# Performance work log

Measured on AMD Instinct MI355X. Metric: run time of the kernel, lower is better.

## Reference

```python
import jax, jax.numpy as jnp
import numpy as np

V, E, H, M, B, S = 32000, 512, 1024, 256, 2, 1024
GC = 24  # smear_gate_channels = min(24, embedding_dim)


def setup_inputs() -> dict:
    key = jax.random.key(0)
    ks = jax.random.split(key, 20)
    s = 0.02
    return {
        "input_ids": jax.random.randint(ks[0], (B, S), 0, V),
        "emb": jax.random.normal(ks[1], (V, E)) * s,
        "W_ih": jax.random.normal(ks[2], (3 * H, E)) * s,
        "W_hh": jax.random.normal(ks[3], (3 * H, H)) * s,
        "b_ih": jax.random.normal(ks[4], (3 * H,)) * s,
        "b_hh": jax.random.normal(ks[5], (3 * H,)) * s,
        "Wq": jax.random.normal(ks[6], (M, H)) * s,
        "bq": jax.random.normal(ks[7], (M,)) * s,
        "Wk": jax.random.normal(ks[8], (M, H)) * s,
        "bk": jax.random.normal(ks[9], (M,)) * s,
        "Wg": jax.random.normal(ks[10], (1, H)) * s,
        "bg": jax.random.normal(ks[11], (1,)) * s,
        "Whe": jax.random.normal(ks[12], (E, H)) * s,
        "bhe": jax.random.normal(ks[13], (E,)) * s,
        "out_bias": jax.random.normal(ks[14], (V,)) * s,
        "memory_scale": jnp.float32(6.0),
        "smear_W": jax.random.normal(ks[15], (1, GC)) * s,
        "smear_lambda": jax.random.normal(ks[16], (1,)) * 0.1,
    }


def forward(input_ids, emb, W_ih, W_hh, b_ih, b_hh, Wq, bq, Wk, bk, Wg, bg,
            Whe, bhe, out_bias, memory_scale, smear_W, smear_lambda):
    x = emb[input_ids]  # (B,S,E)
    # smear: gated copy of previous token embedding into current
    sg = smear_lambda * jax.nn.sigmoid(x[:, 1:, :GC] @ smear_W.T)  # (B,S-1,1)
    x = jnp.concatenate([x[:, :1], x[:, 1:] + sg * x[:, :-1]], axis=1)
    # GRU (PyTorch gate order r,z,n); precompute input projections
    xg = x @ W_ih.T + b_ih  # (B,S,3H)

    def step(h, xg_t):
        xr, xz, xn = jnp.split(xg_t, 3, axis=-1)
        hg = h @ W_hh.T + b_hh
        hr, hz, hn = jnp.split(hg, 3, axis=-1)
        r = jax.nn.sigmoid(xr + hr)
        z = jax.nn.sigmoid(xz + hz)
        n = jnp.tanh(xn + r * hn)
        h_new = (1.0 - z) * n + z * h
        return h_new, h_new

    h0 = jnp.zeros((x.shape[0], H), dtype=x.dtype)
    _, states = jax.lax.scan(step, h0, jnp.swapaxes(xg, 0, 1))
    states = jnp.swapaxes(states, 0, 1)  # (B,S,H); dropout is identity at eval
    # tied output projection
    base_logits = (states @ Whe.T + bhe) @ emb.T + out_bias  # (B,S,V)
    q = states @ Wq.T + bq  # (B,S,M)
    k = states @ Wk.T + bk
    scores = jnp.einsum("bsm,btm->bst", q, k) / jnp.sqrt(jnp.float32(M))
    mask = jnp.tril(jnp.ones((S, S), dtype=bool), k=-1)[None]  # (1,S,S)
    scores = jnp.where(mask, scores, jnp.finfo(scores.dtype).min)
    attn = jax.nn.softmax(scores, axis=-1) * mask
    attn = attn / jnp.maximum(attn.sum(axis=-1, keepdims=True), 1e-6)
    g = jax.nn.sigmoid(states @ Wg.T + bg)  # (B,S,1)
    gated = attn * (g * memory_scale)  # (B,S,S)
    # scatter_add gated attention into vocab logits at input_ids positions
    b_idx = jnp.arange(B)[:, None, None]
    s_idx = jnp.arange(S)[None, :, None]
    v_idx = input_ids[:, None, :]  # broadcasts to (B,S,S)
    base_logits = base_logits.at[b_idx, s_idx, v_idx].add(gated)
    return base_logits


def reference(input_ids, emb, W_ih, W_hh, b_ih, b_hh, Wq, bq, Wk, bk, Wg, bg,
              Whe, bhe, out_bias, memory_scale, smear_W, smear_lambda):
    return forward(input_ids, emb, W_ih, W_hh, b_ih, b_hh, Wq, bq, Wk, bk,
                   Wg, bg, Whe, bhe, out_bias, memory_scale, smear_W, smear_lambda)
```

## Files before the change

### kernel.cpp

```cpp
#include <hip/hip_runtime.h>
#include <stdint.h>

#define V_ 32000
#define E_ 512
#define H_ 1024
#define M_ 256
#define B_ 2
#define S_ 1024
#define GC_ 24

typedef unsigned short u16;
typedef unsigned int u32;
typedef unsigned long long u64;

typedef __attribute__((ext_vector_type(8))) short short8;
typedef __attribute__((ext_vector_type(4))) float floatx4;
typedef __attribute__((ext_vector_type(2))) float floatx2;
typedef __attribute__((ext_vector_type(2))) _Float16 halfx2;

__device__ __forceinline__ float bf2f(u16 u){ return __uint_as_float(((u32)u) << 16); }
__device__ __forceinline__ float bflo(u32 u){ return __uint_as_float(u << 16); }
__device__ __forceinline__ float bfhi(u32 u){ return __uint_as_float(u & 0xffff0000u); }
__device__ __forceinline__ u16 f2bf(float f){
  u32 u = __float_as_uint(f);
  u32 r = (u + 0x7fffu + ((u >> 16) & 1u)) >> 16;
  return (u16)r;
}
__device__ __forceinline__ float sigm(float x){ return 1.f / (1.f + __expf(-x)); }

__device__ __forceinline__ float dot2f16(u32 a, u32 b, float c){
#if __has_builtin(__builtin_amdgcn_fdot2)
  return __builtin_amdgcn_fdot2(__builtin_bit_cast(halfx2, a),
                                __builtin_bit_cast(halfx2, b), c, false);
#else
  halfx2 av = __builtin_bit_cast(halfx2, a);
  halfx2 bv = __builtin_bit_cast(halfx2, b);
  return fmaf((float)av.y, (float)bv.y, fmaf((float)av.x, (float)bv.x, c));
#endif
}

__device__ __forceinline__ void gload_lds16(const void* g, void* l){
  __builtin_amdgcn_global_load_lds(
      (const __attribute__((address_space(1))) void*)g,
      (__attribute__((address_space(3))) void*)l, 16, 0, 0);
}

__global__ __launch_bounds__(64) void detect_kernel(const u32* __restrict__ emb,
    int* __restrict__ flag, float* __restrict__ scal,
    const void* __restrict__ lam, const void* __restrict__ ms)
{
  int lane = threadIdx.x;
  int c = 0;
  for (int i = lane; i < 256; i += 64){
    u32 w = emb[i];
    float a = fabsf(__uint_as_float((w & 0xffffu) << 16));
    if (a > 1e-5f && a < 1.0f) c++;
  }
  #pragma unroll
  for (int o = 32; o; o >>= 1) c += __shfl_down(c, o, 64);
  if (lane == 0){
    int isf32 = (c < 128) ? 1 : 0;
    *flag = isf32;
    if (isf32) scal[0] = ((const float*)lam)[0];
    else {
      float v = bf2f(((const u16*)lam)[0]);
      scal[0] = (fabsf(v) <= 4.0f) ? v : ((const float*)lam)[0];
    }
    if (isf32) scal[1] = ((const float*)ms)[0];
    else {
      u16 a = ((const u16*)ms)[0];
      float v = bf2f(a);
      scal[1] = (a != 0 && fabsf(v) > 1e-4f && fabsf(v) < 1e4f) ? v : ((const float*)ms)[0];
    }
  }
}

struct ConvArgs { const void* s[15]; };

#define CONV_TOTAL 22191385
__global__ __launch_bounds__(256) void convall_kernel(ConvArgs a, char* __restrict__ ws,
                                                      const int* __restrict__ flag)
{
  static const int    ns[15]    = {16384000, 1572864, 3145728, 262144, 262144, 1024,
                                   524288, 3072, 3072, 256, 256, 1, 512, 32000, 24};
  static const size_t doffs[15] = {33280, 32801280, 35947008, 42238464, 42762752,
                                   43287040, 43289088, 44337664, 44343808, 44349952,
                                   44350464, 44350976, 44351232, 44352256, 44416512};
  int gid = blockIdx.x * 256 + threadIdx.x;
  if (gid >= CONV_TOTAL) return;
  int isf32 = *flag;
  int seg = -1, r = gid;
  #pragma unroll
  for (int k = 0; k < 15; k++){
    if (seg < 0){ if (r < ns[k]) seg = k; else r -= ns[k]; }
  }
  const void* src = a.s[seg];
  u16* dst = (u16*)(ws + doffs[seg]);
  if (seg == 2){
    float v = isf32 ? ((const float*)src)[r] : bf2f(((const u16*)src)[r]);
    dst[r] = __builtin_bit_cast(u16, (_Float16)v);
  } else {
    dst[r] = isf32 ? f2bf(((const float*)src)[r]) : ((const u16*)src)[r];
  }
}

__global__ __launch_bounds__(64) void smear_kernel(const int* __restrict__ ids,
    const u16* __restrict__ emb, const u16* __restrict__ smW,
    const float* __restrict__ scal, u16* __restrict__ xs)
{
  int row = blockIdx.x;
  int t = row & (S_ - 1);
  int lane = threadIdx.x;
  int id = ids[row];
  const u16* er = emb + (size_t)id * E_;
  float sg = 0.f;
  if (t > 0){
    float p = 0.f;
    if (lane < GC_) p = bf2f(er[lane]) * bf2f(smW[lane]);
    #pragma unroll
    for (int o = 32; o; o >>= 1) p += __shfl_down(p, o, 64);
    float dot = __shfl(p, 0, 64);
    sg = scal[0] * sigm(dot);
  }
  uint4 cur = ((const uint4*)er)[lane];
  uint4 outv = cur;
  if (t > 0){
    const u16* ep = emb + (size_t)ids[row - 1] * E_;
    uint4 prv = ((const uint4*)ep)[lane];
    const u16* cu = (const u16*)&cur;
    const u16* pu = (const u16*)&prv;
    u16* po = (u16*)&outv;
    #pragma unroll
    for (int j = 0; j < 8; j++) po[j] = f2bf(bf2f(cu[j]) + sg * bf2f(pu[j]));
  }
  ((uint4*)(xs + (size_t)row * E_))[lane] = outv;
}

template<bool OUT_BF16>
__global__ __launch_bounds__(256) void gemm_bt(
    const u16* __restrict__ A, const u16* __restrict__ Bm,
    const u16* __restrict__ bias, void* __restrict__ Cout,
    int K, int Ndim)
{
  int wave = threadIdx.x >> 6, lane = threadIdx.x & 63;
  int wm = wave >> 1, wn = wave & 1;
  int m0 = blockIdx.y * 128 + wm * 64;
  int n0 = blockIdx.x * 128 + wn * 64;
  int lrow = lane & 15, lq = lane >> 4;
  floatx4 acc[4][4];
  #pragma unroll
  for (int i = 0; i < 4; i++)
    #pragma unroll
    for (int j = 0; j < 4; j++) acc[i][j] = (floatx4)0.f;
  const u16* Ab = A + (size_t)(m0 + lrow) * K + lq * 8;
  const u16* Bb = Bm + (size_t)(n0 + lrow) * K + lq * 8;
  for (int k0 = 0; k0 < K; k0 += 32){
    short8 af[4], bfr[4];
    #pragma unroll
    for (int tt = 0; tt < 4; tt++)
      af[tt] = *(const short8*)(Ab + (size_t)tt * 16 * K + k0);
    #pragma unroll
    for (int tt = 0; tt < 4; tt++)
      bfr[tt] = *(const short8*)(Bb + (size_t)tt * 16 * K + k0);
    #pragma unroll
    for (int im = 0; im < 4; im++)
      #pragma unroll
      for (int in = 0; in < 4; in++)
        acc[im][in] = __builtin_amdgcn_mfma_f32_16x16x32_bf16(af[im], bfr[in], acc[im][in], 0, 0, 0);
  }
  #pragma unroll
  for (int in = 0; in < 4; in++){
    int n = n0 + in * 16 + lrow;
    float bv = bf2f(bias[n]);
    #pragma unroll
    for (int im = 0; im < 4; im++){
      int mb = m0 + im * 16 + lq * 4;
      #pragma unroll
      for (int r = 0; r < 4; r++){
        float v = acc[im][in][r] + bv;
        size_t off = (size_t)(mb + r) * Ndim + n;
        if (OUT_BF16) ((u16*)Cout)[off] = f2bf(v);
        else          ((float*)Cout)[off] = v;
      }
    }
  }
}

__global__ __launch_bounds__(256) void gemm_v(
    const u16* __restrict__ A, const u16* __restrict__ Bm,
    const u16* __restrict__ bias, float* __restrict__ Cout,
    int K, int Ndim)
{
  __shared__ u16 la[128 * 32];
  __shared__ u16 lb[128 * 32];
  int wave = threadIdx.x >> 6, lane = threadIdx.x & 63;
  int wm = wave >> 1, wn = wave & 1;
  int tm0 = blockIdx.x * 128, tn0 = blockIdx.y * 128;
  int m0 = tm0 + wm * 64;
  int n0 = tn0 + wn * 64;
  int lrow = lane & 15, lq = lane >> 4;
  floatx4 acc[4][4];
  #pragma unroll
  for (int i = 0; i < 4; i++)
    #pragma unroll
    for (int j = 0; j < 4; j++) acc[i][j] = (floatx4)0.f;

  const int o = wave * 1024 + lane * 16;
  for (int k0 = 0; k0 < K; k0 += 32){
    #pragma unroll
    for (int j = 0; j < 2; j++){
      int oo = o + j * 4096;
      int row = oo >> 6;
      int ce  = (oo & 63) >> 1;
      gload_lds16(&A[(size_t)(tm0 + row) * K + k0 + ce],  &la[(wave * 1024 + j * 4096) >> 1]);
      gload_lds16(&Bm[(size_t)(tn0 + row) * K + k0 + ce], &lb[(wave * 1024 + j * 4096) >> 1]);
    }
    __syncthreads();
    short8 af[4], bfr[4];
    #pragma unroll
    for (int tt = 0; tt < 4; tt++)
      af[tt] = *(const short8*)&la[(wm * 64 + tt * 16 + lrow) * 32 + lq * 8];
    #pragma unroll
    for (int tt = 0; tt < 4; tt++)
      bfr[tt] = *(const short8*)&lb[(wn * 64 + tt * 16 + lrow) * 32 + lq * 8];
    #pragma unroll
    for (int im = 0; im < 4; im++)
      #pragma unroll
      for (int in = 0; in < 4; in++)
        acc[im][in] = __builtin_amdgcn_mfma_f32_16x16x32_bf16(af[im], bfr[in], acc[im][in], 0, 0, 0);
    __syncthreads();
  }
  #pragma unroll
  for (int in = 0; in < 4; in++){
    int n = n0 + in * 16 + lrow;
    float bv = bf2f(bias[n]);
    #pragma unroll
    for (int im = 0; im < 4; im++){
      int mb = m0 + im * 16 + lq * 4;
      #pragma unroll
      for (int r = 0; r < 4; r++)
        Cout[(size_t)(mb + r) * Ndim + n] = acc[im][in][r] + bv;
    }
  }
}

__global__ __launch_bounds__(1024) void gru_kernel(
    const float* __restrict__ xg, const u16* __restrict__ W_hh,
    const u16* __restrict__ b_hh, u32* __restrict__ hslot,
    u16* __restrict__ states, const int* __restrict__ ids, int* __restrict__ sorted)
{
  __shared__ int arr[S_];
  if (blockIdx.x >= 64){
    int b = blockIdx.x - 64, tid = threadIdx.x;
    arr[tid] = (ids[b * S_ + tid] << 11) | tid;
    __syncthreads();
    for (int k = 2; k <= S_; k <<= 1){
      for (int j = k >> 1; j > 0; j >>= 1){
        int ixj = tid ^ j;
        if (ixj > tid){
          int a = arr[tid], c = arr[ixj];
          bool dir = (tid & k) == 0;
          if (dir ? (a > c) : (a < c)){ arr[tid] = c; arr[ixj] = a; }
        }
        __syncthreads();
      }
    }
    sorted[b * S_ + tid] = arr[tid];
    return;
  }

  const int b = blockIdx.x >> 5;
  const int ibase = (blockIdx.x & 31) * 32;
  const int tid = threadIdx.x;
  const int kg = tid >> 5;
  const int il = tid & 31;
  const int i = ibase + il;
  const int w = tid >> 6;

  __shared__ u32   lds_hpk[2][H_ / 2];
  __shared__ float red[3][16][32];

  uint4 Wv[3][4];
  #pragma unroll
  for (int g = 0; g < 3; g++){
    const uint4* p = (const uint4*)(W_hh + ((size_t)(g * H_ + i)) * H_ + kg * 32);
    #pragma unroll
    for (int q = 0; q < 4; q++) Wv[g][q] = p[q];
  }

  float ho = 0.f, xr0 = 0.f, xz0 = 0.f, xn0 = 0.f, bh0 = 0.f, bh1 = 0.f, bh2 = 0.f;
  if (tid < 32){
    bh0 = bf2f(b_hh[ibase + tid]);
    bh1 = bf2f(b_hh[H_ + ibase + tid]);
    bh2 = bf2f(b_hh[2 * H_ + ibase + tid]);
    size_t base = ((size_t)(b * S_)) * 3072 + ibase + tid;
    xr0 = xg[base]; xz0 = xg[base + 1024]; xn0 = xg[base + 2048];
  }

  for (int t = 0; t < S_; t++){
    const int p = t & 1;
    if (tid < 512){
      const u64* rp = (const u64*)(hslot + ((size_t)((p ^ 1) * B_ + b)) * H_) + tid;
      const u32 tg = (u32)t;
      u64 u0;
      do {
        u0 = __hip_atomic_load(rp, __ATOMIC_RELAXED, __HIP_MEMORY_SCOPE_AGENT);
      } while ((((u32)(u0 >> 16) & 0xffffu) != tg) | (((u32)(u0 >> 48)) != tg));
      lds_hpk[p][tid] = ((u32)u0 & 0xffffu) | (((u32)(u0 >> 32)) << 16);
    }
    __syncthreads();
    const u32* hp = &lds_hpk[p][kg * 16];
    float pr = 0.f, pz = 0.f, pn = 0.f;
    #pragma unroll
    for (int q = 0; q < 4; q++){
      uint4 wr = Wv[0][q], wz = Wv[1][q], wn4 = Wv[2][q];
      u32 cr[4] = {wr.x, wr.y, wr.z, wr.w};
      u32 cz[4] = {wz.x, wz.y, wz.z, wz.w};
      u32 cn[4] = {wn4.x, wn4.y, wn4.z, wn4.w};
      #pragma unroll
      for (int e = 0; e < 4; e++){
        u32 h2 = hp[q * 4 + e];
        pr = dot2f16(cr[e], h2, pr);
        pz = dot2f16(cz[e], h2, pz);
        pn = dot2f16(cn[e], h2, pn);
      }
    }
    pr += __shfl_xor(pr, 32, 64);
    pz += __shfl_xor(pz, 32, 64);
    pn += __shfl_xor(pn, 32, 64);
    if ((tid & 63) < 32){
      red[0][w][il] = pr; red[1][w][il] = pz; red[2][w][il] = pn;
    }
    __syncthreads();
    if (tid < 32){
      __builtin_amdgcn_s_setprio(1);
      float hr = 0.f, hz = 0.f, hn = 0.f;
      #pragma unroll
      for (int ww = 0; ww < 16; ww++){
        hr += red[0][ww][tid]; hz += red[1][ww][tid]; hn += red[2][ww][tid];
      }
      float r = sigm(xr0 + hr + bh0);
      float z = sigm(xz0 + hz + bh1);
      float xx = xn0 + r * (hn + bh2);
      float ax = fabsf(xx);
      float et = __expf(-2.f * ax);
      float n = copysignf((1.f - et) * __builtin_amdgcn_rcpf(1.f + et), xx);
      float hnew = (1.f - z) * n + z * ho;
      ho = hnew;
      u16 h16 = __builtin_bit_cast(u16, (_Float16)hnew);
      u32 tgv = (((u32)(t + 1)) << 16) | (u32)h16;
      __hip_atomic_store(&hslot[((size_t)(p * B_ + b)) * H_ + ibase + tid], tgv,
                         __ATOMIC_RELAXED, __HIP_MEMORY_SCOPE_AGENT);
      __builtin_amdgcn_s_setprio(0);
      states[((size_t)(b * S_ + t)) * H_ + ibase + tid] = f2bf(hnew);
      if (t + 1 < S_){
        size_t base = ((size_t)(b * S_ + t + 1)) * 3072 + ibase + tid;
        xr0 = xg[base]; xz0 = xg[base + 1024]; xn0 = xg[base + 2048];
      }
    }
  }
}

__global__ __launch_bounds__(256) void gk_kernel(const u16* __restrict__ states,
    const u16* __restrict__ Wg, const u16* __restrict__ bg, float* __restrict__ gws)
{
  int row = blockIdx.x * 4 + (threadIdx.x >> 6);
  int lane = threadIdx.x & 63;
  const u16* sr = states + (size_t)row * H_;
  float p = 0.f;
  #pragma unroll
  for (int j = 0; j < 16; j++){
    int c = j * 64 + lane;
    p += bf2f(sr[c]) * bf2f(Wg[c]);
  }
  #pragma unroll
  for (int o = 32; o; o >>= 1) p += __shfl_xor(p, o, 64);
  if (lane == 0) gws[row] = sigm(p + bf2f(bg[0]));
}

__global__ __launch_bounds__(256) void attn_scatter_kernel(
    const float* __restrict__ scores, const float* __restrict__ gws,
    const float* __restrict__ scal, const int* __restrict__ sorted,
    float* __restrict__ out)
{
  int s = blockIdx.x, b = blockIdx.y;
  if (s == 0) return;
  int tid = threadIdx.x;
  __shared__ float grow[S_];
  __shared__ int   sb[S_];
  __shared__ float rbm[4], rbs[4];
  const float* srow = scores + ((size_t)(b * S_ + s)) * S_;
  #pragma unroll
  for (int r = 0; r < 4; r++) sb[tid + 256 * r] = sorted[b * S_ + tid + 256 * r];
  float myS[4];
  float lmax = -1e30f;
  #pragma unroll
  for (int r = 0; r < 4; r++){
    int t = tid + 256 * r;
    if (t < s){
      float d = srow[t] * 0.0625f;
      myS[r] = d;
      lmax = fmaxf(lmax, d);
    }
  }
  #pragma unroll
  for (int o = 32; o; o >>= 1) lmax = fmaxf(lmax, __shfl_xor(lmax, o, 64));
  if ((tid & 63) == 0) rbm[tid >> 6] = lmax;
  __syncthreads();
  float gmax = fmaxf(fmaxf(rbm[0], rbm[1]), fmaxf(rbm[2], rbm[3]));
  float lsum = 0.f;
  #pragma unroll
  for (int r = 0; r < 4; r++){
    int t = tid + 256 * r;
    if (t < s){ myS[r] = __expf(myS[r] - gmax); lsum += myS[r]; }
  }
  #pragma unroll
  for (int o = 32; o; o >>= 1) lsum += __shfl_xor(lsum, o, 64);
  if ((tid & 63) == 0) rbs[tid >> 6] = lsum;
  __syncthreads();
  float gsum = rbs[0] + rbs[1] + rbs[2] + rbs[3];
  float fac = gws[b * S_ + s] * scal[1] / gsum;
  #pragma unroll
  for (int r = 0; r < 4; r++){
    int t = tid + 256 * r;
    if (t < s) grow[t] = myS[r] * fac;
  }
  __syncthreads();
  float* orow = out + ((size_t)(b * S_ + s)) * V_;
  #pragma unroll
  for (int r = 0; r < 4; r++){
    int e = tid + 256 * r;
    int pk = sb[e];
    int v = pk >> 11;
    if (e > 0 && (sb[e - 1] >> 11) == v) continue;
    float sum = 0.f; bool any = false;
    for (int j = e; j < S_; j++){
      int pj = sb[j];
      if ((pj >> 11) != v) break;
      int t = pj & 2047;
      if (t < s){ sum += grow[t]; any = true; }
    }
    if (any) orow[v] += sum;
  }
}

extern "C" void kernel_launch(void* const* d_in, const int* in_sizes, int n_in,
                              void* d_out, int out_size, void* d_ws, size_t ws_size,
                              hipStream_t stream)
{
  const int*  ids   = (const int*)d_in[0];
  const void* emb   = d_in[1];
  const void* W_ih  = d_in[2];
  const void* W_hh  = d_in[3];
  const void* b_ih  = d_in[4];
  const void* b_hh  = d_in[5];
  const void* Wq    = d_in[6];
  const void* bq    = d_in[7];
  const void* Wk    = d_in[8];
  const void* bk    = d_in[9];
  const void* Wg    = d_in[10];
  const void* bg    = d_in[11];
  const void* Whe   = d_in[12];
  const void* bhe   = d_in[13];
  const void* obias = d_in[14];
  const void* ms    = d_in[15];
  const void* smW   = d_in[16];
  const void* lam   = d_in[17];
  (void)in_sizes; (void)n_in; (void)out_size; (void)ws_size;

  char* ws = (char*)d_ws;
  int*   flag   = (int*)(ws + 0);
  float* scal   = (float*)(ws + 256);
  u32*   hslot  = (u32*)(ws + 512);
  u16*   zbias  = (u16*)(ws + 16896);
  u16*   c_emb  = (u16*)(ws + 33280);
  u16*   c_Wih  = (u16*)(ws + 32801280);
  u16*   c_Whh  = (u16*)(ws + 35947008);
  u16*   c_Wq   = (u16*)(ws + 42238464);
  u16*   c_Wk   = (u16*)(ws + 42762752);
  u16*   c_Wg   = (u16*)(ws + 43287040);
  u16*   c_Whe  = (u16*)(ws + 43289088);
  u16*   c_bih  = (u16*)(ws + 44337664);
  u16*   c_bhh  = (u16*)(ws + 44343808);
  u16*   c_bq   = (u16*)(ws + 44349952);
  u16*   c_bk   = (u16*)(ws + 44350464);
  u16*   c_bg   = (u16*)(ws + 44350976);
  u16*   c_bhe  = (u16*)(ws + 44351232);
  u16*   c_ob   = (u16*)(ws + 44352256);
  u16*   c_smW  = (u16*)(ws + 44416512);
  u16*   xs     = (u16*)(ws + 44416768);
  float* xg     = (float*)(ws + 46513920);
  u16*   states = (u16*)(ws + 71679744);
  u16*   hs     = (u16*)(ws + 75874048);
  u16*   qb     = (u16*)(ws + 77971200);
  u16*   kb     = (u16*)(ws + 79019776);
  float* gws    = (float*)(ws + 80068352);
  int*   sorted = (int*)(ws + 88465152);
  float* scores = xg;
  float* out = (float*)d_out;

  hipMemsetAsync(hslot, 0, 16384, stream);
  hipMemsetAsync(zbias, 0, 2048, stream);
  detect_kernel<<<dim3(1), dim3(64), 0, stream>>>((const u32*)emb, flag, scal, lam, ms);

  ConvArgs ca;
  ca.s[0] = emb;  ca.s[1] = W_ih; ca.s[2] = W_hh; ca.s[3] = Wq;   ca.s[4] = Wk;
  ca.s[5] = Wg;   ca.s[6] = Whe;  ca.s[7] = b_ih; ca.s[8] = b_hh; ca.s[9] = bq;
  ca.s[10] = bk;  ca.s[11] = bg;  ca.s[12] = bhe; ca.s[13] = obias; ca.s[14] = smW;
  convall_kernel<<<dim3((CONV_TOTAL + 255) / 256), dim3(256), 0, stream>>>(ca, ws, flag);

  smear_kernel<<<dim3(B_ * S_), dim3(64), 0, stream>>>(ids, c_emb, c_smW, scal, xs);
  gemm_bt<false><<<dim3(3072 / 128, 2048 / 128), dim3(256), 0, stream>>>(xs, c_Wih, c_bih, (void*)xg, E_, 3072);
  gru_kernel<<<dim3(66), dim3(1024), 0, stream>>>(xg, c_Whh, c_bhh, hslot, states, ids, sorted);
  gemm_bt<true><<<dim3(512 / 128, 16), dim3(256), 0, stream>>>(states, c_Whe, c_bhe, (void*)hs, H_, 512);
  gemm_bt<true><<<dim3(256 / 128, 16), dim3(256), 0, stream>>>(states, c_Wq, c_bq, (void*)qb, H_, 256);
  gemm_bt<true><<<dim3(256 / 128, 16), dim3(256), 0, stream>>>(states, c_Wk, c_bk, (void*)kb, H_, 256);
  gemm_bt<false><<<dim3(S_ / 128, S_ / 128), dim3(256), 0, stream>>>(qb, kb, zbias, (void*)scores, M_, S_);
  gemm_bt<false><<<dim3(S_ / 128, S_ / 128), dim3(256), 0, stream>>>(qb + (size_t)S_ * M_, kb + (size_t)S_ * M_,
                                                                     zbias, (void*)(scores + (size_t)S_ * S_), M_, S_);
  gk_kernel<<<dim3(512), dim3(256), 0, stream>>>(states, c_Wg, c_bg, gws);
  gemm_v<<<dim3(16, V_ / 128), dim3(256), 0, stream>>>(hs, c_emb, c_ob, out, E_, V_);
  attn_scatter_kernel<<<dim3(S_, B_), dim3(256), 0, stream>>>(scores, gws, scal, sorted, out);
}
```

Before: 2.484 ms.

## Fuse GRU with downstream GEMMs in persistent megakernel overlapping via progress counters

Merges the GRU recurrence, bitonic sort, output-projection, Q/K projection, vocab-logit and score GEMMs into one persistent kernel. The GRU blocks bump per-128-step counters, and 190 extra worker blocks wait on those counters to run dependent GEMM tiles while the recurrence is still going. The goal is to hide the large vocab GEMM and the projections behind the latency-bound sequential GRU. In exchange, the GEMM tiles now read operands straight from global memory with no LDS staging, and the workers spin-wait, which risks contending with the GRU blocks for CUs and memory bandwidth. It also relies on every block being co-resident to avoid deadlock.

```diff
diff --git a/kernel.cpp b/kernel.cpp
--- a/kernel.cpp
+++ b/kernel.cpp
@@ -39,12 +39,6 @@
 #endif
 }
 
-__device__ __forceinline__ void gload_lds16(const void* g, void* l){
-  __builtin_amdgcn_global_load_lds(
-      (const __attribute__((address_space(1))) void*)g,
-      (__attribute__((address_space(3))) void*)l, 16, 0, 0);
-}
-
 __global__ __launch_bounds__(64) void detect_kernel(const u32* __restrict__ emb,
     int* __restrict__ flag, float* __restrict__ scal,
     const void* __restrict__ lam, const void* __restrict__ ms)
@@ -186,16 +180,11 @@
   }
 }
 
-__global__ __launch_bounds__(256) void gemm_v(
-    const u16* __restrict__ A, const u16* __restrict__ Bm,
-    const u16* __restrict__ bias, float* __restrict__ Cout,
-    int K, int Ndim)
-{
-  __shared__ u16 la[128 * 32];
-  __shared__ u16 lb[128 * 32];
-  int wave = threadIdx.x >> 6, lane = threadIdx.x & 63;
+__device__ void tile_gemm(const u16* __restrict__ A, const u16* __restrict__ Bm,
+                          const u16* __restrict__ bias, void* __restrict__ Cout,
+                          int K, int Ndim, int tm0, int tn0, int wave, int lane, int outbf)
+{
   int wm = wave >> 1, wn = wave & 1;
-  int tm0 = blockIdx.x * 128, tn0 = blockIdx.y * 128;
   int m0 = tm0 + wm * 64;
   int n0 = tn0 + wn * 64;
   int lrow = lane & 15, lq = lane >> 4;
@@ -204,31 +193,21 @@
   for (int i = 0; i < 4; i++)
     #pragma unroll
     for (int j = 0; j < 4; j++) acc[i][j] = (floatx4)0.f;
-
-  const int o = wave * 1024 + lane * 16;
+  const u16* Ab = A + (size_t)(m0 + lrow) * K + lq * 8;
+  const u16* Bb = Bm + (size_t)(n0 + lrow) * K + lq * 8;
   for (int k0 = 0; k0 < K; k0 += 32){
-    #pragma unroll
-    for (int j = 0; j < 2; j++){
-      int oo = o + j * 4096;
-      int row = oo >> 6;
-      int ce  = (oo & 63) >> 1;
-      gload_lds16(&A[(size_t)(tm0 + row) * K + k0 + ce],  &la[(wave * 1024 + j * 4096) >> 1]);
-      gload_lds16(&Bm[(size_t)(tn0 + row) * K + k0 + ce], &lb[(wave * 1024 + j * 4096) >> 1]);
-    }
-    __syncthreads();
     short8 af[4], bfr[4];
     #pragma unroll
     for (int tt = 0; tt < 4; tt++)
-      af[tt] = *(const short8*)&la[(wm * 64 + tt * 16 + lrow) * 32 + lq * 8];
+      af[tt] = *(const short8*)(Ab + (size_t)tt * 16 * K + k0);
     #pragma unroll
     for (int tt = 0; tt < 4; tt++)
-      bfr[tt] = *(const short8*)&lb[(wn * 64 + tt * 16 + lrow) * 32 + lq * 8];
+      bfr[tt] = *(const short8*)(Bb + (size_t)tt * 16 * K + k0);
     #pragma unroll
     for (int im = 0; im < 4; im++)
       #pragma unroll
       for (int in = 0; in < 4; in++)
         acc[im][in] = __builtin_amdgcn_mfma_f32_16x16x32_bf16(af[im], bfr[in], acc[im][in], 0, 0, 0);
-    __syncthreads();
   }
   #pragma unroll
   for (int in = 0; in < 4; in++){
@@ -238,40 +217,110 @@
     for (int im = 0; im < 4; im++){
       int mb = m0 + im * 16 + lq * 4;
       #pragma unroll
-      for (int r = 0; r < 4; r++)
-        Cout[(size_t)(mb + r) * Ndim + n] = acc[im][in][r] + bv;
-    }
-  }
-}
-
-__global__ __launch_bounds__(1024) void gru_kernel(
-    const float* __restrict__ xg, const u16* __restrict__ W_hh,
-    const u16* __restrict__ b_hh, u32* __restrict__ hslot,
-    u16* __restrict__ states, const int* __restrict__ ids, int* __restrict__ sorted)
-{
+      for (int r = 0; r < 4; r++){
+        float v = acc[im][in][r] + bv;
+        size_t off = (size_t)(mb + r) * Ndim + n;
+        if (outbf) ((u16*)Cout)[off] = f2bf(v);
+        else       ((float*)Cout)[off] = v;
+      }
+    }
+  }
+}
+
+struct MegaArgs {
+  const float* xg; const u16* Whh; const u16* bhh; u32* hslot; u16* states;
+  const int* ids; int* sorted;
+  const u16* Whe; const u16* bhe; u16* hs;
+  const u16* Wq;  const u16* bq;  u16* qb;
+  const u16* Wk;  const u16* bk;  u16* kb;
+  const u16* emb; const u16* ob;  float* out;
+  const u16* zbias; float* scores;
+  u32* ctr;
+};
+
+__global__ __launch_bounds__(1024) void mega_kernel(MegaArgs a)
+{
+  const int tid = threadIdx.x;
+
   __shared__ int arr[S_];
-  if (blockIdx.x >= 64){
-    int b = blockIdx.x - 64, tid = threadIdx.x;
-    arr[tid] = (ids[b * S_ + tid] << 11) | tid;
+  if (blockIdx.x >= 64 && blockIdx.x < 66){
+    int b = blockIdx.x - 64;
+    arr[tid] = (a.ids[b * S_ + tid] << 11) | tid;
     __syncthreads();
     for (int k = 2; k <= S_; k <<= 1){
       for (int j = k >> 1; j > 0; j >>= 1){
         int ixj = tid ^ j;
         if (ixj > tid){
-          int a = arr[tid], c = arr[ixj];
+          int x = arr[tid], c = arr[ixj];
           bool dir = (tid & k) == 0;
-          if (dir ? (a > c) : (a < c)){ arr[tid] = c; arr[ixj] = a; }
+          if (dir ? (x > c) : (x < c)){ arr[tid] = c; arr[ixj] = x; }
         }
         __syncthreads();
       }
     }
-    sorted[b * S_ + tid] = arr[tid];
+    a.sorted[b * S_ + tid] = arr[tid];
+    return;
+  }
+
+  if (blockIdx.x >= 66){
+    const int wid = blockIdx.x - 66;
+    const int qt = tid >> 8;
+    const int qtid = tid & 255;
+    const int wave = qtid >> 6, lane = qtid & 63;
+    u32* prog = a.ctr;
+    u32* hsd  = a.ctr + 16;
+    u32* qkvt = a.ctr + 32;
+    for (int q = wid; q < 1072; q += 190){
+      int type, mt = 0, nq = 0, sbb = 0, si = 0, sj0 = 0;
+      if (q < 1040){
+        int c = q / 130, r = q - c * 130;
+        if (r < 2){ type = 0; mt = c + 8 * r; }
+        else if (r < 4){ type = 1; mt = c + 8 * (r - 2); }
+        else { type = 2; int rr = r - 4; mt = c + 8 * (rr / 63); nq = rr - (rr / 63) * 63; }
+      } else {
+        type = 3; int r = q - 1040; sbb = r >> 4;
+        int qq = r & 15; si = qq >> 1; sj0 = (qq & 1) * 4;
+      }
+      if (tid == 0){
+        if (type <= 1){
+          while (__hip_atomic_load(&prog[mt], __ATOMIC_ACQUIRE, __HIP_MEMORY_SCOPE_AGENT) < 32u)
+            __builtin_amdgcn_s_sleep(8);
+        } else if (type == 2){
+          while (__hip_atomic_load(&hsd[mt], __ATOMIC_ACQUIRE, __HIP_MEMORY_SCOPE_AGENT) == 0u)
+            __builtin_amdgcn_s_sleep(8);
+        } else {
+          while (__hip_atomic_load(qkvt, __ATOMIC_ACQUIRE, __HIP_MEMORY_SCOPE_AGENT) < 16u)
+            __builtin_amdgcn_s_sleep(8);
+        }
+      }
+      __syncthreads();
+      if (type == 0){
+        tile_gemm(a.states, a.Whe, a.bhe, a.hs, H_, 512, mt * 128, qt * 128, wave, lane, 1);
+      } else if (type == 1){
+        if (qt < 2) tile_gemm(a.states, a.Wq, a.bq, a.qb, H_, M_, mt * 128, qt * 128, wave, lane, 1);
+        else        tile_gemm(a.states, a.Wk, a.bk, a.kb, H_, M_, mt * 128, (qt - 2) * 128, wave, lane, 1);
+      } else if (type == 2){
+        int ntile = nq * 4 + qt;
+        if (ntile < 250)
+          tile_gemm(a.hs, a.emb, a.ob, a.out, E_, V_, mt * 128, ntile * 128, wave, lane, 0);
+      } else {
+        int j = sj0 + qt;
+        tile_gemm(a.qb + (size_t)sbb * S_ * M_, a.kb + (size_t)sbb * S_ * M_, a.zbias,
+                  a.scores + (size_t)sbb * S_ * S_, M_, S_, si * 128, j * 128, wave, lane, 0);
+      }
+      __syncthreads();
+      if (tid == 0){
+        if (type == 0)
+          __hip_atomic_store(&hsd[mt], 1u, __ATOMIC_RELEASE, __HIP_MEMORY_SCOPE_AGENT);
+        else if (type == 1)
+          __hip_atomic_fetch_add(qkvt, 1u, __ATOMIC_RELEASE, __HIP_MEMORY_SCOPE_AGENT);
+      }
+    }
     return;
   }
 
   const int b = blockIdx.x >> 5;
   const int ibase = (blockIdx.x & 31) * 32;
-  const int tid = threadIdx.x;
   const int kg = tid >> 5;
   const int il = tid & 31;
   const int i = ibase + il;
@@ -283,24 +332,24 @@
   uint4 Wv[3][4];
   #pragma unroll
   for (int g = 0; g < 3; g++){
-    const uint4* p = (const uint4*)(W_hh + ((size_t)(g * H_ + i)) * H_ + kg * 32);
+    const uint4* p = (const uint4*)(a.Whh + ((size_t)(g * H_ + i)) * H_ + kg * 32);
     #pragma unroll
     for (int q = 0; q < 4; q++) Wv[g][q] = p[q];
   }
 
   float ho = 0.f, xr0 = 0.f, xz0 = 0.f, xn0 = 0.f, bh0 = 0.f, bh1 = 0.f, bh2 = 0.f;
   if (tid < 32){
-    bh0 = bf2f(b_hh[ibase + tid]);
-    bh1 = bf2f(b_hh[H_ + ibase + tid]);
-    bh2 = bf2f(b_hh[2 * H_ + ibase + tid]);
+    bh0 = bf2f(a.bhh[ibase + tid]);
+    bh1 = bf2f(a.bhh[H_ + ibase + tid]);
+    bh2 = bf2f(a.bhh[2 * H_ + ibase + tid]);
     size_t base = ((size_t)(b * S_)) * 3072 + ibase + tid;
-    xr0 = xg[base]; xz0 = xg[base + 1024]; xn0 = xg[base + 2048];
+    xr0 = a.xg[base]; xz0 = a.xg[base + 1024]; xn0 = a.xg[base + 2048];
   }
 
   for (int t = 0; t < S_; t++){
     const int p = t & 1;
     if (tid < 512){
-      const u64* rp = (const u64*)(hslot + ((size_t)((p ^ 1) * B_ + b)) * H_) + tid;
+      const u64* rp = (const u64*)(a.hslot + ((size_t)((p ^ 1) * B_ + b)) * H_) + tid;
       const u32 tg = (u32)t;
       u64 u0;
       do {
@@ -349,13 +398,16 @@
       ho = hnew;
       u16 h16 = __builtin_bit_cast(u16, (_Float16)hnew);
       u32 tgv = (((u32)(t + 1)) << 16) | (u32)h16;
-      __hip_atomic_store(&hslot[((size_t)(p * B_ + b)) * H_ + ibase + tid], tgv,
+      __hip_atomic_store(&a.hslot[((size_t)(p * B_ + b)) * H_ + ibase + tid], tgv,
                          __ATOMIC_RELAXED, __HIP_MEMORY_SCOPE_AGENT);
       __builtin_amdgcn_s_setprio(0);
-      states[((size_t)(b * S_ + t)) * H_ + ibase + tid] = f2bf(hnew);
+      a.states[((size_t)(b * S_ + t)) * H_ + ibase + tid] = f2bf(hnew);
+      if (((t + 1) & 127) == 0 && tid == 0)
+        __hip_atomic_fetch_add(&a.ctr[b * 8 + (t >> 7)], 1u,
+                               __ATOMIC_RELEASE, __HIP_MEMORY_SCOPE_AGENT);
       if (t + 1 < S_){
         size_t base = ((size_t)(b * S_ + t + 1)) * 3072 + ibase + tid;
-        xr0 = xg[base]; xz0 = xg[base + 1024]; xn0 = xg[base + 2048];
+        xr0 = a.xg[base]; xz0 = a.xg[base + 1024]; xn0 = a.xg[base + 2048];
       }
     }
   }
@@ -473,6 +525,7 @@
   float* scal   = (float*)(ws + 256);
   u32*   hslot  = (u32*)(ws + 512);
   u16*   zbias  = (u16*)(ws + 16896);
+  u32*   ctr    = (u32*)(ws + 20480);
   u16*   c_emb  = (u16*)(ws + 33280);
   u16*   c_Wih  = (u16*)(ws + 32801280);
   u16*   c_Whh  = (u16*)(ws + 35947008);
@@ -501,6 +554,7 @@
 
   hipMemsetAsync(hslot, 0, 16384, stream);
   hipMemsetAsync(zbias, 0, 2048, stream);
+  hipMemsetAsync(ctr, 0, 256, stream);
   detect_kernel<<<dim3(1), dim3(64), 0, stream>>>((const u32*)emb, flag, scal, lam, ms);
 
   ConvArgs ca;
@@ -511,14 +565,18 @@
 
   smear_kernel<<<dim3(B_ * S_), dim3(64), 0, stream>>>(ids, c_emb, c_smW, scal, xs);
   gemm_bt<false><<<dim3(3072 / 128, 2048 / 128), dim3(256), 0, stream>>>(xs, c_Wih, c_bih, (void*)xg, E_, 3072);
-  gru_kernel<<<dim3(66), dim3(1024), 0, stream>>>(xg, c_Whh, c_bhh, hslot, states, ids, sorted);
-  gemm_bt<true><<<dim3(512 / 128, 16), dim3(256), 0, stream>>>(states, c_Whe, c_bhe, (void*)hs, H_, 512);
-  gemm_bt<true><<<dim3(256 / 128, 16), dim3(256), 0, stream>>>(states, c_Wq, c_bq, (void*)qb, H_, 256);
-  gemm_bt<true><<<dim3(256 / 128, 16), dim3(256), 0, stream>>>(states, c_Wk, c_bk, (void*)kb, H_, 256);
-  gemm_bt<false><<<dim3(S_ / 128, S_ / 128), dim3(256), 0, stream>>>(qb, kb, zbias, (void*)scores, M_, S_);
-  gemm_bt<false><<<dim3(S_ / 128, S_ / 128), dim3(256), 0, stream>>>(qb + (size_t)S_ * M_, kb + (size_t)S_ * M_,
-                                                                     zbias, (void*)(scores + (size_t)S_ * S_), M_, S_);
+
+  MegaArgs ma;
+  ma.xg = xg;        ma.Whh = c_Whh;  ma.bhh = c_bhh;  ma.hslot = hslot;  ma.states = states;
+  ma.ids = ids;      ma.sorted = sorted;
+  ma.Whe = c_Whe;    ma.bhe = c_bhe;  ma.hs = hs;
+  ma.Wq = c_Wq;      ma.bq = c_bq;    ma.qb = qb;
+  ma.Wk = c_Wk;      ma.bk = c_bk;    ma.kb = kb;
+  ma.emb = c_emb;    ma.ob = c_ob;    ma.out = out;
+  ma.zbias = zbias;  ma.scores = scores;
+  ma.ctr = ctr;
+  mega_kernel<<<dim3(256), dim3(1024), 0, stream>>>(ma);
+
   gk_kernel<<<dim3(512), dim3(256), 0, stream>>>(states, c_Wg, c_bg, gws);
-  gemm_v<<<dim3(16, V_ / 128), dim3(256), 0, stream>>>(hs, c_emb, c_ob, out, E_, V_);
   attn_scatter_kernel<<<dim3(S_, B_), dim3(256), 0, stream>>>(scores, gws, scal, sorted, out);
 }
```

New measurement: 4.721 ms. +90.1%, slower.
